# Performance work log

Measured on AMD Instinct MI355X. Metric: run time of the kernel, lower is better.

Reference implementation:

```python
import jax, jax.numpy as jnp
import numpy as np

L2_REG = 0.01  # config['l2_reg']


def setup_inputs() -> dict:
    key = jax.random.key(0)
    k1, k2, k3, k4 = jax.random.split(key, 4)
    N = 16384
    risk_pred = jax.random.normal(k1, (N, 1), dtype=jnp.float32)
    y = jax.random.uniform(k2, (N, 1), dtype=jnp.float32)  # survival times
    e = jax.random.randint(k3, (N, 1), 0, 2, dtype=jnp.int32)  # event indicator
    W = jax.random.normal(k4, (512, 256), dtype=jnp.float32)  # model weight for L2 reg
    return {"risk_pred": risk_pred, "y": y, "e": e, "W": W}


def reference(risk_pred, y, e, W):
    # mask[i, j] = 1 if y[j] <= y[i] else 0  (torch: mask[y.T - y > 0] = 0)
    mask = (y.T - y <= 0).astype(risk_pred.dtype)  # (N, N)
    exp_r = jnp.exp(risk_pred)                      # (N, 1), broadcasts over rows
    num = jnp.sum(exp_r * mask, axis=0)             # (N,) risk-set weighted sum per column
    den = jnp.sum(mask, axis=0)                     # (N,) risk-set size per column
    log_loss = jnp.log(num / den).reshape(-1, 1)    # (N, 1)
    ef = e.astype(risk_pred.dtype)
    neg_log_loss = -jnp.sum((risk_pred - log_loss) * ef) / jnp.sum(ef)
    l2_loss = L2_REG * jnp.linalg.norm(W)           # Regularization(order=2)
    return neg_log_loss + l2_loss
```

## Files before the change

kernel.cpp:

```cpp
#include <hip/hip_runtime.h>

#define L2_REG 0.01f
#define NBIN 1024
#define MAXB 64


__global__ __launch_bounds__(256) void cox_hist(const float* __restrict__ rp,
                                                const float* __restrict__ y,
                                                const float* __restrict__ W,
                                                int* __restrict__ cnt,
                                                float* __restrict__ sum,
                                                float* __restrict__ by,
                                                float* __restrict__ be,
                                                float* __restrict__ wpart) {
    const int b = blockIdx.x;
    if (b < 64) {
        const int i = b * 256 + threadIdx.x;
        const float yi = y[i];
        const float ei = __expf(rp[i]);
        int bin = (int)(yi * (float)NBIN);
        bin = min(max(bin, 0), NBIN - 1);
        atomicAdd(&sum[bin], ei);
        const int pos = atomicAdd(&cnt[bin], 1);
        if (pos < MAXB) {
            by[bin * MAXB + pos] = yi;
            be[bin * MAXB + pos] = ei;
        }
    } else {
        __shared__ float l[4];
        const float4* W4 = reinterpret_cast<const float4*>(W) + (b - 64) * 512;
        float s = 0.f;
#pragma unroll
        for (int k = 0; k < 2; ++k) {
            float4 w = W4[k * 256 + threadIdx.x];
            s = fmaf(w.x, w.x, s); s = fmaf(w.y, w.y, s);
            s = fmaf(w.z, w.z, s); s = fmaf(w.w, w.w, s);
        }
#pragma unroll
        for (int off = 32; off; off >>= 1) s += __shfl_down(s, off, 64);
        const int lane = threadIdx.x & 63, wave = threadIdx.x >> 6;
        if (lane == 0) l[wave] = s;
        __syncthreads();
        if (threadIdx.x == 0) wpart[b - 64] = l[0] + l[1] + l[2] + l[3];
    }
}

__global__ __launch_bounds__(1024) void cox_scan(const int* __restrict__ cnt,
                                                 const float* __restrict__ sum,
                                                 const float* __restrict__ wpart,
                                                 float* __restrict__ sufc,
                                                 float* __restrict__ sufs,
                                                 float* __restrict__ acc,
                                                 int* __restrict__ cnt2) {
    const int t = threadIdx.x;
    const int rt = (NBIN - 1) - t;
    const int lane = t & 63, wave = t >> 6;
    float c = (float)cnt[rt];
    float s = sum[rt];
#pragma unroll
    for (int off = 1; off < 64; off <<= 1) {
        const float pc = __shfl_up(c, off, 64);
        const float ps = __shfl_up(s, off, 64);
        if (lane >= off) { c += pc; s += ps; }
    }
    __shared__ float wc[16], wsm[16];
    if (lane == 63) { wc[wave] = c; wsm[wave] = s; }
    __syncthreads();
    if (t < 16) {
        float vc = wc[t], vs = wsm[t];
#pragma unroll
        for (int off = 1; off < 16; off <<= 1) {
            const float pc = __shfl_up(vc, off, 64);
            const float ps = __shfl_up(vs, off, 64);
            if (lane >= off) { vc += pc; vs += ps; }
        }
        wc[t] = vc; wsm[t] = vs;
    }
    __syncthreads();
    if (wave > 0) { c += wc[wave - 1]; s += wsm[wave - 1]; }
    sufc[rt] = c;
    sufs[rt] = s;
    if (t == 0) {
        sufc[NBIN] = 0.f; sufs[NBIN] = 0.f;
        acc[0] = 0.f; acc[1] = 0.f; cnt2[0] = 0;
    }
    if (t < 64) {
        float wv = wpart[t];
#pragma unroll
        for (int off = 32; off; off >>= 1) wv += __shfl_down(wv, off, 64);
        if (t == 0) acc[2] = wv;
    }
}

__global__ __launch_bounds__(64) void cox_terms(const float* __restrict__ rp,
                                                const float* __restrict__ y,
                                                const int* __restrict__ e,
                                                const int* __restrict__ cnt,
                                                const float* __restrict__ by,
                                                const float* __restrict__ be,
                                                const float* __restrict__ sufc,
                                                const float* __restrict__ sufs,
                                                float* __restrict__ acc,
                                                int* __restrict__ cnt2,
                                                float* __restrict__ out) {
    const int j = blockIdx.x * 64 + threadIdx.x;
    const float yj = y[j];
    int bin = (int)(yj * (float)NBIN);
    bin = min(max(bin, 0), NBIN - 1);
    float den = sufc[bin + 1];
    float num = sufs[bin + 1];
    const int nb = min(cnt[bin], MAXB);
    const float4* by4 = reinterpret_cast<const float4*>(by + bin * MAXB);
    const float4* be4 = reinterpret_cast<const float4*>(be + bin * MAXB);
    for (int p = 0; p < nb; p += 4) {
        const float4 yv = by4[p >> 2];
        const float4 ev = be4[p >> 2];
        const float m0 = (yv.x >= yj) ? 1.f : 0.f;
        const float m1 = ((p + 1 < nb) && (yv.y >= yj)) ? 1.f : 0.f;
        const float m2 = ((p + 2 < nb) && (yv.z >= yj)) ? 1.f : 0.f;
        const float m3 = ((p + 3 < nb) && (yv.w >= yj)) ? 1.f : 0.f;
        den += m0; num = fmaf(m0, ev.x, num);
        den += m1; num = fmaf(m1, ev.y, num);
        den += m2; num = fmaf(m2, ev.z, num);
        den += m3; num = fmaf(m3, ev.w, num);
    }
    const float ef = (float)e[j];
    float term = (rp[j] - __logf(num / den)) * ef;
    float es = ef;
#pragma unroll
    for (int off = 32; off; off >>= 1) {
        term += __shfl_down(term, off, 64);
        es   += __shfl_down(es,   off, 64);
    }
    if (threadIdx.x != 0) return;
    atomicAdd(&acc[0], term);
    atomicAdd(&acc[1], es);
    __threadfence();
    if (atomicAdd(cnt2, 1) == 255) {
        const float a0 = atomicAdd(&acc[0], 0.f);
        const float a1 = atomicAdd(&acc[1], 0.f);
        out[0] = -a0 / a1 + L2_REG * sqrtf(acc[2]);
    }
}

extern "C" void kernel_launch(void* const* d_in, const int* in_sizes, int n_in,
                              void* d_out, int out_size, void* d_ws, size_t ws_size,
                              hipStream_t stream) {
    const float* rp = (const float*)d_in[0];
    const float* y  = (const float*)d_in[1];
    const int*   e  = (const int*)d_in[2];
    const float* W  = (const float*)d_in[3];

    int*   cnt   = (int*)d_ws;
    float* sum   = (float*)(cnt + NBIN);
    float* by    = sum + NBIN;
    float* be    = by + NBIN * MAXB;
    float* sufc  = be + NBIN * MAXB;
    float* sufs  = sufc + NBIN + 4;
    float* wpart = sufs + NBIN + 4;
    float* acc   = wpart + 64;
    int*   cnt2  = (int*)(acc + 4);

    hipMemsetAsync(d_ws, 0, 2 * NBIN * sizeof(float), stream);

    cox_hist<<<dim3(128), dim3(256), 0, stream>>>(rp, y, W, cnt, sum, by, be, wpart);
    cox_scan<<<dim3(1), dim3(1024), 0, stream>>>(cnt, sum, wpart, sufc, sufs, acc, cnt2);
    cox_terms<<<dim3(256), dim3(64), 0, stream>>>(rp, y, e, cnt, by, be, sufc, sufs,
                                                  acc, cnt2, (float*)d_out);
}
```

Before: 81.84 us.

## Fuse histogram, scan and term kernels into one single-block LDS kernel

Replaces the three kernel launches and the memset with one 1024-thread block that does the histogram, suffix scan and counting-sort bucketing in shared memory, then computes every term there. This removes launch and memset overhead, global atomics and the MAXB bucket cap, which is also a correctness limit in the old code. In exchange all of the work runs on a single CU, and y and rp are read twice from global memory. The block uses about 140KB of LDS, which may exceed the per-workgroup limit on some targets.

```diff
diff --git a/kernel.cpp b/kernel.cpp
--- a/kernel.cpp
+++ b/kernel.cpp
@@ -1,170 +1,136 @@
 #include <hip/hip_runtime.h>
 
 #define L2_REG 0.01f
-#define NBIN 1024
-#define MAXB 64
+#define NTOT 16384
+#define NBIN 2048
+#define NT   1024
 
+__global__ __launch_bounds__(NT) void cox_all(const float* __restrict__ rp,
+                                              const float* __restrict__ y,
+                                              const int* __restrict__ e,
+                                              const float* __restrict__ W,
+                                              float* __restrict__ out) {
+    __shared__ float2 s_ye[NTOT];
+    __shared__ int    s_off[NBIN];
+    __shared__ float  s_suf[NBIN + 1];
+    __shared__ float  s_wred[16], s_tred[16], s_ered[16];
 
-__global__ __launch_bounds__(256) void cox_hist(const float* __restrict__ rp,
-                                                const float* __restrict__ y,
-                                                const float* __restrict__ W,
-                                                int* __restrict__ cnt,
-                                                float* __restrict__ sum,
-                                                float* __restrict__ by,
-                                                float* __restrict__ be,
-                                                float* __restrict__ wpart) {
-    const int b = blockIdx.x;
-    if (b < 64) {
-        const int i = b * 256 + threadIdx.x;
-        const float yi = y[i];
-        const float ei = __expf(rp[i]);
+    const int t = threadIdx.x;
+    const int lane = t & 63, wave = t >> 6;
+
+    s_off[t] = 0; s_off[t + NT] = 0;
+    s_suf[t] = 0.f; s_suf[t + NT] = 0.f;
+    float ws = 0.f;
+    const float4* W4 = reinterpret_cast<const float4*>(W);
+#pragma unroll
+    for (int i = 0; i < 32; ++i) {
+        const float4 w = W4[i * NT + t];
+        ws = fmaf(w.x, w.x, ws); ws = fmaf(w.y, w.y, ws);
+        ws = fmaf(w.z, w.z, ws); ws = fmaf(w.w, w.w, ws);
+    }
+#pragma unroll
+    for (int o = 32; o; o >>= 1) ws += __shfl_down(ws, o, 64);
+    if (lane == 0) s_wred[wave] = ws;
+    __syncthreads();
+
+#pragma unroll
+    for (int i = 0; i < NTOT / NT; ++i) {
+        const int idx = i * NT + t;
+        const float yi = y[idx];
+        const float ei = __expf(rp[idx]);
         int bin = (int)(yi * (float)NBIN);
         bin = min(max(bin, 0), NBIN - 1);
-        atomicAdd(&sum[bin], ei);
-        const int pos = atomicAdd(&cnt[bin], 1);
-        if (pos < MAXB) {
-            by[bin * MAXB + pos] = yi;
-            be[bin * MAXB + pos] = ei;
-        }
-    } else {
-        __shared__ float l[4];
-        const float4* W4 = reinterpret_cast<const float4*>(W) + (b - 64) * 512;
-        float s = 0.f;
+        atomicAdd(&s_off[bin], 1);
+        atomicAdd(&s_suf[bin], ei);
+    }
+    __syncthreads();
+
+    const int   c0  = s_off[2 * t], c1 = s_off[2 * t + 1];
+    const float shi = s_suf[NBIN - 1 - 2 * t], slo = s_suf[NBIN - 2 - 2 * t];
+    int   cp = c0 + c1;
+    float sp = shi + slo;
 #pragma unroll
-        for (int k = 0; k < 2; ++k) {
-            float4 w = W4[k * 256 + threadIdx.x];
-            s = fmaf(w.x, w.x, s); s = fmaf(w.y, w.y, s);
-            s = fmaf(w.z, w.z, s); s = fmaf(w.w, w.w, s);
-        }
-#pragma unroll
-        for (int off = 32; off; off >>= 1) s += __shfl_down(s, off, 64);
-        const int lane = threadIdx.x & 63, wave = threadIdx.x >> 6;
-        if (lane == 0) l[wave] = s;
-        __syncthreads();
-        if (threadIdx.x == 0) wpart[b - 64] = l[0] + l[1] + l[2] + l[3];
+    for (int o = 1; o < 64; o <<= 1) {
+        const int   pc = __shfl_up(cp, o, 64);
+        const float ps = __shfl_up(sp, o, 64);
+        if (lane >= o) { cp += pc; sp += ps; }
     }
-}
-
-__global__ __launch_bounds__(1024) void cox_scan(const int* __restrict__ cnt,
-                                                 const float* __restrict__ sum,
-                                                 const float* __restrict__ wpart,
-                                                 float* __restrict__ sufc,
-                                                 float* __restrict__ sufs,
-                                                 float* __restrict__ acc,
-                                                 int* __restrict__ cnt2) {
-    const int t = threadIdx.x;
-    const int rt = (NBIN - 1) - t;
-    const int lane = t & 63, wave = t >> 6;
-    float c = (float)cnt[rt];
-    float s = sum[rt];
-#pragma unroll
-    for (int off = 1; off < 64; off <<= 1) {
-        const float pc = __shfl_up(c, off, 64);
-        const float ps = __shfl_up(s, off, 64);
-        if (lane >= off) { c += pc; s += ps; }
-    }
-    __shared__ float wc[16], wsm[16];
-    if (lane == 63) { wc[wave] = c; wsm[wave] = s; }
+    if (lane == 63) { s_tred[wave] = (float)cp; s_ered[wave] = sp; }
     __syncthreads();
     if (t < 16) {
-        float vc = wc[t], vs = wsm[t];
+        float vc = s_tred[t], vs = s_ered[t];
 #pragma unroll
-        for (int off = 1; off < 16; off <<= 1) {
-            const float pc = __shfl_up(vc, off, 64);
-            const float ps = __shfl_up(vs, off, 64);
-            if (lane >= off) { vc += pc; vs += ps; }
+        for (int o = 1; o < 16; o <<= 1) {
+            const float pc = __shfl_up(vc, o, 64);
+            const float ps = __shfl_up(vs, o, 64);
+            if (lane >= o) { vc += pc; vs += ps; }
         }
-        wc[t] = vc; wsm[t] = vs;
+        s_tred[t] = vc; s_ered[t] = vs;
     }
     __syncthreads();
-    if (wave > 0) { c += wc[wave - 1]; s += wsm[wave - 1]; }
-    sufc[rt] = c;
-    sufs[rt] = s;
+    const int   ci = cp + (wave ? (int)s_tred[wave - 1] : 0);
+    const float si = sp + (wave ? s_ered[wave - 1] : 0.f);
+    s_off[2 * t]     = ci - c0 - c1;
+    s_off[2 * t + 1] = ci - c1;
+    s_suf[NBIN - 2 - 2 * t] = si;
+    s_suf[NBIN - 1 - 2 * t] = si - slo;
+    if (t == 0) s_suf[NBIN] = 0.f;
+    __syncthreads();
+
+#pragma unroll
+    for (int i = 0; i < NTOT / NT; ++i) {
+        const int idx = i * NT + t;
+        const float yi = y[idx];
+        const float ei = __expf(rp[idx]);
+        int bin = (int)(yi * (float)NBIN);
+        bin = min(max(bin, 0), NBIN - 1);
+        const int pos = atomicAdd(&s_off[bin], 1);
+        s_ye[pos] = make_float2(yi, ei);
+    }
+    __syncthreads();
+
+    float tsum = 0.f, esum = 0.f;
+    for (int i = 0; i < NTOT / NT; ++i) {
+        const int idx = i * NT + t;
+        const float yj = y[idx];
+        int bin = (int)(yj * (float)NBIN);
+        bin = min(max(bin, 0), NBIN - 1);
+        const int k1 = s_off[bin];
+        const int k0 = bin ? s_off[bin - 1] : 0;
+        float den = (float)(NTOT - k1);
+        float num = s_suf[bin + 1];
+        for (int k = k0; k < k1; ++k) {
+            const float2 v = s_ye[k];
+            const float m = (v.x >= yj) ? 1.f : 0.f;
+            den += m;
+            num = fmaf(m, v.y, num);
+        }
+        const float ef = (float)e[idx];
+        tsum = fmaf(ef, rp[idx] - __logf(num / den), tsum);
+        esum += ef;
+    }
+#pragma unroll
+    for (int o = 32; o; o >>= 1) {
+        tsum += __shfl_down(tsum, o, 64);
+        esum += __shfl_down(esum, o, 64);
+    }
+    if (lane == 0) { s_tred[wave] = tsum; s_ered[wave] = esum; }
+    __syncthreads();
     if (t == 0) {
-        sufc[NBIN] = 0.f; sufs[NBIN] = 0.f;
-        acc[0] = 0.f; acc[1] = 0.f; cnt2[0] = 0;
-    }
-    if (t < 64) {
-        float wv = wpart[t];
+        float T_ = 0.f, E_ = 0.f, WS = 0.f;
 #pragma unroll
-        for (int off = 32; off; off >>= 1) wv += __shfl_down(wv, off, 64);
-        if (t == 0) acc[2] = wv;
-    }
-}
-
-__global__ __launch_bounds__(64) void cox_terms(const float* __restrict__ rp,
-                                                const float* __restrict__ y,
-                                                const int* __restrict__ e,
-                                                const int* __restrict__ cnt,
-                                                const float* __restrict__ by,
-                                                const float* __restrict__ be,
-                                                const float* __restrict__ sufc,
-                                                const float* __restrict__ sufs,
-                                                float* __restrict__ acc,
-                                                int* __restrict__ cnt2,
-                                                float* __restrict__ out) {
-    const int j = blockIdx.x * 64 + threadIdx.x;
-    const float yj = y[j];
-    int bin = (int)(yj * (float)NBIN);
-    bin = min(max(bin, 0), NBIN - 1);
-    float den = sufc[bin + 1];
-    float num = sufs[bin + 1];
-    const int nb = min(cnt[bin], MAXB);
-    const float4* by4 = reinterpret_cast<const float4*>(by + bin * MAXB);
-    const float4* be4 = reinterpret_cast<const float4*>(be + bin * MAXB);
-    for (int p = 0; p < nb; p += 4) {
-        const float4 yv = by4[p >> 2];
-        const float4 ev = be4[p >> 2];
-        const float m0 = (yv.x >= yj) ? 1.f : 0.f;
-        const float m1 = ((p + 1 < nb) && (yv.y >= yj)) ? 1.f : 0.f;
-        const float m2 = ((p + 2 < nb) && (yv.z >= yj)) ? 1.f : 0.f;
-        const float m3 = ((p + 3 < nb) && (yv.w >= yj)) ? 1.f : 0.f;
-        den += m0; num = fmaf(m0, ev.x, num);
-        den += m1; num = fmaf(m1, ev.y, num);
-        den += m2; num = fmaf(m2, ev.z, num);
-        den += m3; num = fmaf(m3, ev.w, num);
-    }
-    const float ef = (float)e[j];
-    float term = (rp[j] - __logf(num / den)) * ef;
-    float es = ef;
-#pragma unroll
-    for (int off = 32; off; off >>= 1) {
-        term += __shfl_down(term, off, 64);
-        es   += __shfl_down(es,   off, 64);
-    }
-    if (threadIdx.x != 0) return;
-    atomicAdd(&acc[0], term);
-    atomicAdd(&acc[1], es);
-    __threadfence();
-    if (atomicAdd(cnt2, 1) == 255) {
-        const float a0 = atomicAdd(&acc[0], 0.f);
-        const float a1 = atomicAdd(&acc[1], 0.f);
-        out[0] = -a0 / a1 + L2_REG * sqrtf(acc[2]);
+        for (int w = 0; w < 16; ++w) { T_ += s_tred[w]; E_ += s_ered[w]; WS += s_wred[w]; }
+        out[0] = -T_ / E_ + L2_REG * sqrtf(WS);
     }
 }
 
 extern "C" void kernel_launch(void* const* d_in, const int* in_sizes, int n_in,
                               void* d_out, int out_size, void* d_ws, size_t ws_size,
                               hipStream_t stream) {
-    const float* rp = (const float*)d_in[0];
-    const float* y  = (const float*)d_in[1];
-    const int*   e  = (const int*)d_in[2];
-    const float* W  = (const float*)d_in[3];
-
-    int*   cnt   = (int*)d_ws;
-    float* sum   = (float*)(cnt + NBIN);
-    float* by    = sum + NBIN;
-    float* be    = by + NBIN * MAXB;
-    float* sufc  = be + NBIN * MAXB;
-    float* sufs  = sufc + NBIN + 4;
-    float* wpart = sufs + NBIN + 4;
-    float* acc   = wpart + 64;
-    int*   cnt2  = (int*)(acc + 4);
-
-    hipMemsetAsync(d_ws, 0, 2 * NBIN * sizeof(float), stream);
-
-    cox_hist<<<dim3(128), dim3(256), 0, stream>>>(rp, y, W, cnt, sum, by, be, wpart);
-    cox_scan<<<dim3(1), dim3(1024), 0, stream>>>(cnt, sum, wpart, sufc, sufs, acc, cnt2);
-    cox_terms<<<dim3(256), dim3(64), 0, stream>>>(rp, y, e, cnt, by, be, sufc, sufs,
-                                                  acc, cnt2, (float*)d_out);
+    (void)in_sizes; (void)n_in; (void)out_size; (void)d_ws; (void)ws_size;
+    cox_all<<<dim3(1), dim3(NT), 0, stream>>>((const float*)d_in[0],
+                                              (const float*)d_in[1],
+                                              (const int*)d_in[2],
+                                              (const float*)d_in[3],
+                                              (float*)d_out);
 }
```

Measured after the change: 107.3 us. +31.2%, slower.
